# Performance work log

Measured on AMD Instinct MI355X. Metric: run time of the kernel, lower is better.

## Reference

```python
import jax, jax.numpy as jnp
import numpy as np

EPS = 1e-5
GROUPS = 8
NUM_HEADS = 8


def setup_inputs() -> dict:
    key = jax.random.key(0)
    ks = jax.random.split(key, 6)
    C = 512
    s = 1.0 / np.sqrt(C)
    return {
        "x": jax.random.normal(ks[0], (8, C, 32, 32), dtype=jnp.float32),
        "gn_w": jnp.ones((C,), jnp.float32),
        "gn_b": jnp.zeros((C,), jnp.float32),
        "wq": jax.random.normal(ks[1], (C, C), jnp.float32) * s,
        "bq": jnp.zeros((C,), jnp.float32),
        "wk": jax.random.normal(ks[2], (C, C), jnp.float32) * s,
        "bk": jnp.zeros((C,), jnp.float32),
        "wv": jax.random.normal(ks[3], (C, C), jnp.float32) * s,
        "bv": jnp.zeros((C,), jnp.float32),
        "wp": jax.random.normal(ks[4], (C, C), jnp.float32) * s,
        "bp": jnp.zeros((C,), jnp.float32),
    }


def _group_norm(x, w, b):
    # x: [B, C, H, W]; normalize per group over (C//G, H, W)
    B, C, H, W = x.shape
    xg = x.reshape(B, GROUPS, -1)
    mean = xg.mean(axis=-1, keepdims=True)
    var = xg.var(axis=-1, keepdims=True)
    xn = ((xg - mean) * jax.lax.rsqrt(var + EPS)).reshape(B, C, H, W)
    return xn * w[None, :, None, None] + b[None, :, None, None]


def reference(x, gn_w, gn_b, wq, bq, wk, bk, wv, bv, wp, bp):
    B, C, H, W = x.shape
    n_heads = NUM_HEADS
    d = C // n_heads
    scale = 1.0 / np.sqrt(d)

    x_flat = x.reshape(B, C, H * W).transpose(0, 2, 1)       # [B, S, C]
    xn = _group_norm(x, gn_w, gn_b).reshape(B, C, H * W).transpose(0, 2, 1)

    # torch Linear: y = x @ W.T + b
    q = (xn @ wq.T + bq).reshape(B, H * W, n_heads, d)        # [B, S, h, d]
    k = (xn @ wk.T + bk).reshape(B, H * W, n_heads, d)
    v = (xn @ wv.T + bv).reshape(B, H * W, n_heads, d)

    attn = jnp.einsum("bnhd,bmhd->bhnm", q, k) * scale       # [B, h, S, S]
    attn = jax.nn.softmax(attn, axis=-1)
    out = jnp.einsum("bhnm,bmhd->bnhd", attn, v).reshape(B, H * W, C)
    out = out @ wp.T + bp
    out = out + x_flat
    return out.transpose(0, 2, 1).reshape(B, C, H, W)
```

## Files before the change

### kernel.cpp

```cpp
#include <hip/hip_runtime.h>
#include <stdint.h>

typedef unsigned short u16;
using bf16x8 = __attribute__((ext_vector_type(8))) short;
using f32x4  = __attribute__((ext_vector_type(4))) float;
using f32x16 = __attribute__((ext_vector_type(16))) float;
typedef unsigned int uv2 __attribute__((ext_vector_type(2)));

#define EPS_GN 1e-5f
#define SCL 0.18033688011112042f

__device__ __forceinline__ u16 f2bf(float f) {
  union { float f; uint32_t u; } x; x.f = f;
  uint32_t r = x.u + 0x7FFFu + ((x.u >> 16) & 1u);
  return (u16)(r >> 16);
}

__device__ __forceinline__ void gload_lds16(const void* g, void* l) {
  __builtin_amdgcn_global_load_lds(
      (const __attribute__((address_space(1))) unsigned int*)g,
      (__attribute__((address_space(3))) unsigned int*)l, 16, 0, 0);
}

__device__ __forceinline__ void fence_tile() {
  asm volatile("s_waitcnt vmcnt(0)" ::: "memory");
  __builtin_amdgcn_s_barrier();
  __builtin_amdgcn_sched_barrier(0);
}

__global__ __launch_bounds__(256) void prep(const float* __restrict__ x,
    float* __restrict__ part,
    const float4* __restrict__ wq, const float4* __restrict__ wk,
    const float4* __restrict__ wv, const float4* __restrict__ wp,
    const float* __restrict__ bq, const float* __restrict__ bk,
    const float* __restrict__ bv,
    u16* __restrict__ wqkv, u16* __restrict__ wpb, float* __restrict__ bqkv) {
  if (blockIdx.x < 512) {
    int bg = blockIdx.x >> 3, seg = blockIdx.x & 7;
    const float4* base = (const float4*)(x + (size_t)bg * 65536 + (size_t)seg * 8192);
    float s = 0.f, s2 = 0.f;
    for (int i = threadIdx.x; i < 2048; i += 256) {
      float4 v = base[i];
      s  += v.x + v.y + v.z + v.w;
      s2 += v.x*v.x + v.y*v.y + v.z*v.z + v.w*v.w;
    }
    for (int m = 1; m < 64; m <<= 1) { s += __shfl_xor(s, m); s2 += __shfl_xor(s2, m); }
    __shared__ float red[4][2];
    int wave = threadIdx.x >> 6;
    if ((threadIdx.x & 63) == 0) { red[wave][0] = s; red[wave][1] = s2; }
    __syncthreads();
    if (threadIdx.x == 0) {
      float a = 0.f, b = 0.f;
      for (int w = 0; w < 4; ++w) { a += red[w][0]; b += red[w][1]; }
      part[blockIdx.x * 2] = a; part[blockIdx.x * 2 + 1] = b;
    }
  } else {
    int i = (blockIdx.x - 512) * 256 + threadIdx.x;
    int seg = i >> 16, j = i & 65535;
    const float4* w = (seg == 0) ? wq : (seg == 1) ? wk : (seg == 2) ? wv : wp;
    u16* o = (seg < 3) ? (wqkv + seg * 262144) : wpb;
    float sc = (seg == 0) ? SCL : 1.f;
    float4 v = w[j];
    o[j*4+0] = f2bf(v.x*sc); o[j*4+1] = f2bf(v.y*sc);
    o[j*4+2] = f2bf(v.z*sc); o[j*4+3] = f2bf(v.w*sc);
    if (i < 1536) bqkv[i] = (i < 512) ? bq[i]*SCL : (i < 1024) ? bk[i-512] : bv[i-1024];
  }
}

__global__ __launch_bounds__(256) void gn_apply(const float* __restrict__ x,
    const float* __restrict__ part, const float* __restrict__ w,
    const float* __restrict__ bb, u16* __restrict__ xn) {
  __shared__ float t[32][33];
  int s0 = blockIdx.x * 32, c0 = blockIdx.y * 32, b = blockIdx.z;
  int g = c0 >> 6;
  float s = 0.f, s2 = 0.f;
  for (int q = 0; q < 8; ++q) {
    s  += part[((b*8+g)*8 + q)*2];
    s2 += part[((b*8+g)*8 + q)*2 + 1];
  }
  float mean = s * (1.f/65536.f);
  float rstd = rsqrtf(s2 * (1.f/65536.f) - mean*mean + EPS_GN);
  for (int i = 0; i < 4; ++i) {
    int c = c0 + threadIdx.y + i * 8;
    float v = x[((size_t)b*512 + c)*1024 + s0 + threadIdx.x];
    t[threadIdx.y + i*8][threadIdx.x] = (v - mean) * rstd * w[c] + bb[c];
  }
  __syncthreads();
  for (int i = 0; i < 4; ++i) {
    int sdx = s0 + threadIdx.y + i * 8;
    xn[((size_t)b*1024 + sdx)*512 + c0 + threadIdx.x] = f2bf(t[threadIdx.x][threadIdx.y + i*8]);
  }
}

__global__ __launch_bounds__(256) void qkv_gemm(const u16* __restrict__ X,
    const u16* __restrict__ W, const float* __restrict__ bias,
    u16* __restrict__ qkb, u16* __restrict__ vP) {
  __shared__ __align__(16) u16 As[2*64*64];
  __shared__ __align__(16) u16 Bs[2*128*64];
  const int K = 512;
  int m0 = (blockIdx.x & 127) * 64, n0 = (blockIdx.x >> 7) * 128;
  int t = threadIdx.x, lane = t & 63, wave = t >> 6;
  int wm = wave >> 1, wn = wave & 1;
  int lr = lane & 15, lg = lane >> 4;
  f32x4 acc[2][4] = {};

  auto stage = [&](int k0, int bufi) {
    u16* Ab = As + bufi * 4096;
    u16* Bb = Bs + bufi * 8192;
#pragma unroll
    for (int c = 0; c < 2; ++c) {
      int chunk = wave * 2 + c;
      int e = chunk * 512 + lane * 8;
      int r = e >> 6, col = e & 63;
      int scol = col ^ ((r & 7) << 3);
      gload_lds16(X + (size_t)(m0 + r) * K + k0 + scol, (char*)Ab + chunk * 1024);
    }
#pragma unroll
    for (int c = 0; c < 4; ++c) {
      int chunk = wave * 4 + c;
      int e = chunk * 512 + lane * 8;
      int r = e >> 6, col = e & 63;
      int scol = col ^ ((r & 7) << 3);
      gload_lds16(W + (size_t)(n0 + r) * K + k0 + scol, (char*)Bb + chunk * 1024);
    }
  };

  stage(0, 0);
  fence_tile();
  int buf = 0;
  for (int k0 = 0; k0 < K; k0 += 64) {
    if (k0 + 64 < K) stage(k0 + 64, buf ^ 1);
    const char* Ab = (const char*)(As + buf * 4096);
    const char* Bb = (const char*)(Bs + buf * 8192);
    bf16x8 af[2][2], bfr[4][2];
#pragma unroll
    for (int kk = 0; kk < 2; ++kk) {
      int ca = kk * 64 + lg * 16;
#pragma unroll
      for (int i = 0; i < 2; ++i) {
        int ra = wm * 32 + i * 16 + lr;
        af[i][kk] = *(const bf16x8*)(Ab + ((ra * 128 + ca) ^ ((ra & 7) << 4)));
      }
#pragma unroll
      for (int j = 0; j < 4; ++j) {
        int rb = wn * 64 + j * 16 + lr;
        bfr[j][kk] = *(const bf16x8*)(Bb + ((rb * 128 + ca) ^ ((rb & 7) << 4)));
      }
    }
    __builtin_amdgcn_s_setprio(1);
#pragma unroll
    for (int kk = 0; kk < 2; ++kk)
#pragma unroll
      for (int i = 0; i < 2; ++i)
#pragma unroll
        for (int j = 0; j < 4; ++j)
          acc[i][j] = __builtin_amdgcn_mfma_f32_16x16x32_bf16(af[i][kk], bfr[j][kk], acc[i][j], 0, 0, 0);
    __builtin_amdgcn_s_setprio(0);
    fence_tile();
    buf ^= 1;
  }
  if (n0 < 1024) {
    for (int i = 0; i < 2; ++i)
      for (int j = 0; j < 4; ++j) {
        int col = n0 + wn * 64 + j * 16 + lr;
        float bv = bias[col];
        int rowb = m0 + wm * 32 + i * 16 + lg * 4;
        for (int r = 0; r < 4; ++r)
          qkb[(size_t)(rowb + r) * 1024 + col] = f2bf(acc[i][j][r] + bv);
      }
  } else {
    for (int i = 0; i < 2; ++i)
      for (int j = 0; j < 4; ++j) {
        int col = n0 + wn * 64 + j * 16 + lr;
        float bv = bias[col];
        int rowb = m0 + wm * 32 + i * 16 + lg * 4;
        int colV = col - 1024;
        int h  = colV >> 6, dl = colV & 63;
        int dt = dl >> 5,  lqv = dl & 31;
        int bb2 = rowb >> 10, s_in = rowb & 1023;
        int tile = s_in >> 6, kvl = s_in & 63;
        int cg = kvl >> 4, hiv = (kvl >> 3) & 1, j0 = kvl & 7;
        int ii = dt * 4 + cg, lv = hiv * 32 + lqv;
        size_t u16off = ((size_t)((h * 8 + bb2) * 16 + tile)) * 4096 + (ii * 64 + lv) * 8 + j0;
        unsigned p0, p1;
        float v0 = acc[i][j][0] + bv, v1 = acc[i][j][1] + bv;
        float v2 = acc[i][j][2] + bv, v3 = acc[i][j][3] + bv;
        asm("v_cvt_pk_bf16_f32 %0, %1, %2" : "=v"(p0) : "v"(v0), "v"(v1));
        asm("v_cvt_pk_bf16_f32 %0, %1, %2" : "=v"(p1) : "v"(v2), "v"(v3));
        uint2 pk; pk.x = p0; pk.y = p1;
        *(uint2*)(vP + u16off) = pk;
      }
  }
}

__global__ __launch_bounds__(256) void proj_gemm(const u16* __restrict__ Wt,
    const u16* __restrict__ X, const float* __restrict__ bias,
    const float* __restrict__ resid, float* __restrict__ Out) {
  __shared__ __align__(16) u16 As[2*128*64];
  __shared__ __align__(16) u16 Bs[2*64*64];
  const int K = 512;
  int m0 = blockIdx.x * 64, n0 = blockIdx.y * 128;
  int t = threadIdx.x, lane = t & 63, wave = t >> 6;
  int wm = wave >> 1, wn = wave & 1;
  int lr = lane & 15, lg = lane >> 4;
  f32x4 acc[4][2] = {};

  auto stage = [&](int k0, int bufi) {
    u16* Ab = As + bufi * 8192;
    u16* Bb = Bs + bufi * 4096;
#pragma unroll
    for (int c = 0; c < 4; ++c) {
      int chunk = wave * 4 + c;
      int e = chunk * 512 + lane * 8;
      int r = e >> 6, col = e & 63;
      int scol = col ^ ((r & 7) << 3);
      gload_lds16(Wt + (size_t)(n0 + r) * K + k0 + scol, (char*)Ab + chunk * 1024);
    }
#pragma unroll
    for (int c = 0; c < 2; ++c) {
      int chunk = wave * 2 + c;
      int e = chunk * 512 + lane * 8;
      int r = e >> 6, col = e & 63;
      int scol = col ^ ((r & 7) << 3);
      gload_lds16(X + (size_t)(m0 + r) * K + k0 + scol, (char*)Bb + chunk * 1024);
    }
  };

  stage(0, 0);
  fence_tile();
  int buf = 0;
  for (int k0 = 0; k0 < K; k0 += 64) {
    if (k0 + 64 < K) stage(k0 + 64, buf ^ 1);
    const char* Ab = (const char*)(As + buf * 8192);
    const char* Bb = (const char*)(Bs + buf * 4096);
    bf16x8 af[4][2], bfr[2][2];
#pragma unroll
    for (int kk = 0; kk < 2; ++kk) {
      int ca = kk * 64 + lg * 16;
#pragma unroll
      for (int i = 0; i < 4; ++i) {
        int ra = wm * 64 + i * 16 + lr;
        af[i][kk] = *(const bf16x8*)(Ab + ((ra * 128 + ca) ^ ((ra & 7) << 4)));
      }
#pragma unroll
      for (int j = 0; j < 2; ++j) {
        int rb = wn * 32 + j * 16 + lr;
        bfr[j][kk] = *(const bf16x8*)(Bb + ((rb * 128 + ca) ^ ((rb & 7) << 4)));
      }
    }
    __builtin_amdgcn_s_setprio(1);
#pragma unroll
    for (int kk = 0; kk < 2; ++kk)
#pragma unroll
      for (int i = 0; i < 4; ++i)
#pragma unroll
        for (int j = 0; j < 2; ++j)
          acc[i][j] = __builtin_amdgcn_mfma_f32_16x16x32_bf16(af[i][kk], bfr[j][kk], acc[i][j], 0, 0, 0);
    __builtin_amdgcn_s_setprio(0);
    fence_tile();
    buf ^= 1;
  }
  for (int i = 0; i < 4; ++i)
    for (int j = 0; j < 2; ++j) {
      int mcol = m0 + wn * 32 + j * 16 + lr;
      for (int r = 0; r < 4; ++r) {
        int nrow = n0 + wm * 64 + i * 16 + lg * 4 + r;
        float v = acc[i][j][r] + bias[nrow];
        size_t b = (size_t)(mcol >> 10); int s = mcol & 1023;
        size_t addr = (b * 512 + nrow) * 1024 + s;
        Out[addr] = v + resid[addr];
      }
    }
}

__global__ __launch_bounds__(512, 4) void attn_fwd(const u16* __restrict__ qk,
    const u16* __restrict__ vP, u16* __restrict__ o) {
  __shared__ __align__(16) u16 smem[26624];
  int bh = blockIdx.x, qb = blockIdx.y;
  int b = bh >> 3, h = bh & 7;
  int t = threadIdx.x, lane = t & 63, wave = t >> 6;
  int half = wave >> 2, wq4 = wave & 3;
  int lq = lane & 31, hi = lane >> 5;
  int qrow0 = qb * 128 + wq4 * 32;
  const u16* qp = qk + (size_t)(b * 1024 + qrow0 + lq) * 1024 + h * 64 + hi * 8;
  bf16x8 qf[4];
#pragma unroll
  for (int s = 0; s < 4; ++s) qf[s] = *(const bf16x8*)(qp + s * 16);
  float li = 0.f;
  f32x16 ot[2] = {};
  int kvbase = half * 512;
  const u16* vb = vP + ((size_t)((h * 8 + b) * 16 + half * 8)) * 4096 + (size_t)lane * 8;

  auto stage = [&](int ti, int bufi) {
    u16* Kb = smem + (half * 2 + bufi) * 4096;
    int kv = kvbase + ti * 64;
#pragma unroll
    for (int c = 0; c < 2; ++c) {
      int chunk = wq4 * 2 + c;
      int e = chunk * 512 + lane * 8;
      int r = e >> 6, col = e & 63;
      int scol = col ^ ((r & 7) << 3);
      gload_lds16(qk + (size_t)(b * 1024 + kv + r) * 1024 + 512 + h * 64 + scol,
                  (char*)Kb + chunk * 1024);
    }
  };

  stage(0, 0);
  fence_tile();
  int buf = 0;
  for (int ti = 0; ti < 8; ++ti) {
    if (ti < 7) stage(ti + 1, buf ^ 1);
    const char* Kb = (const char*)(smem + (half * 2 + buf) * 4096);
    f32x16 st[2];
#pragma unroll
    for (int n2 = 0; n2 < 2; ++n2) {
      int rk = n2 * 32 + lq;
      f32x16 z = {};
      __builtin_amdgcn_s_setprio(1);
#pragma unroll
      for (int s = 0; s < 4; ++s) {
        bf16x8 kf = *(const bf16x8*)(Kb + ((rk * 128 + s * 32 + hi * 16) ^ ((rk & 7) << 4)));
        z = __builtin_amdgcn_mfma_f32_32x32x16_bf16(kf, qf[s], z, 0, 0, 0);
      }
      __builtin_amdgcn_s_setprio(0);
      st[n2] = z;
    }
    float sm[16];
#pragma unroll
    for (int r = 0; r < 16; ++r) {
      float e0 = __builtin_amdgcn_exp2f(st[0][r]);
      float e1 = __builtin_amdgcn_exp2f(st[1][r]);
      st[0][r] = e0; st[1][r] = e1;
      sm[r] = e0 + e1;
    }
#pragma unroll
    for (int s = 8; s > 0; s >>= 1)
#pragma unroll
      for (int r = 0; r < s; ++r) sm[r] += sm[r + s];
    li += sm[0] + __shfl_xor(sm[0], 32);
    bf16x8 fr[4];
#pragma unroll
    for (int n2 = 0; n2 < 2; ++n2) {
#pragma unroll
      for (int c = 0; c < 2; ++c) {
        unsigned W0, W1, W2, W3;
        asm("v_cvt_pk_bf16_f32 %0, %1, %2" : "=v"(W0) : "v"(st[n2][8*c+0]), "v"(st[n2][8*c+1]));
        asm("v_cvt_pk_bf16_f32 %0, %1, %2" : "=v"(W1) : "v"(st[n2][8*c+2]), "v"(st[n2][8*c+3]));
        asm("v_cvt_pk_bf16_f32 %0, %1, %2" : "=v"(W2) : "v"(st[n2][8*c+4]), "v"(st[n2][8*c+5]));
        asm("v_cvt_pk_bf16_f32 %0, %1, %2" : "=v"(W3) : "v"(st[n2][8*c+6]), "v"(st[n2][8*c+7]));
        uv2 r02 = __builtin_amdgcn_permlane32_swap(W0, W2, false, false);
        uv2 r13 = __builtin_amdgcn_permlane32_swap(W1, W3, false, false);
        union { unsigned u[4]; bf16x8 v; } f;
        f.u[0] = r02[0]; f.u[1] = r13[0]; f.u[2] = r02[1]; f.u[3] = r13[1];
        fr[n2 * 2 + c] = f.v;
      }
    }
    bf16x8 vr[8];
#pragma unroll
    for (int i = 0; i < 8; ++i) vr[i] = *(const bf16x8*)(vb + ti * 4096 + i * 512);
    __builtin_amdgcn_s_setprio(1);
#pragma unroll
    for (int cg = 0; cg < 4; ++cg)
#pragma unroll
      for (int dt = 0; dt < 2; ++dt)
        ot[dt] = __builtin_amdgcn_mfma_f32_32x32x16_bf16(vr[dt * 4 + cg], fr[cg], ot[dt], 0, 0, 0);
    __builtin_amdgcn_s_setprio(0);
    fence_tile();
    buf ^= 1;
  }
  float* cbuf = (float*)smem;
  float* wreg = cbuf + wq4 * 2176;
  if (half == 0) {
#pragma unroll
    for (int dt = 0; dt < 2; ++dt)
#pragma unroll
      for (int r = 0; r < 16; ++r)
        wreg[(dt * 16 + r) * 64 + lane] = ot[dt][r];
    wreg[2048 + lane] = li;
  }
  __syncthreads();
  if (half == 1) {
    float inv = 1.f / (wreg[2048 + lane] + li);
    u16* wb = smem + 18432 + wq4 * 2048;
#pragma unroll
    for (int dt = 0; dt < 2; ++dt)
#pragma unroll
      for (int g = 0; g < 4; ++g) {
        float v0 = (wreg[(dt*16 + 4*g+0)*64 + lane] + ot[dt][4*g+0]) * inv;
        float v1 = (wreg[(dt*16 + 4*g+1)*64 + lane] + ot[dt][4*g+1]) * inv;
        float v2 = (wreg[(dt*16 + 4*g+2)*64 + lane] + ot[dt][4*g+2]) * inv;
        float v3 = (wreg[(dt*16 + 4*g+3)*64 + lane] + ot[dt][4*g+3]) * inv;
        unsigned p0, p1;
        asm("v_cvt_pk_bf16_f32 %0, %1, %2" : "=v"(p0) : "v"(v0), "v"(v1));
        asm("v_cvt_pk_bf16_f32 %0, %1, %2" : "=v"(p1) : "v"(v2), "v"(v3));
        int ch = dt * 8 + 2 * g + hi;
        int pos = ch ^ ((lq & 7) << 1);
        uint2 wv; wv.x = p0; wv.y = p1;
        *(uint2*)((char*)wb + lq * 128 + pos * 8) = wv;
      }
    int q2 = lane >> 1, j0 = lane & 1;
#pragma unroll
    for (int jj = 0; jj < 4; ++jj) {
      int j = j0 + jj * 2;
      uint4 val = *(const uint4*)((const char*)wb + q2 * 128 + ((j ^ (q2 & 7)) << 4));
      *(uint4*)(o + (size_t)(b * 1024 + qrow0 + q2) * 512 + h * 64 + j * 8) = val;
    }
  }
}

extern "C" void kernel_launch(void* const* d_in, const int* in_sizes, int n_in,
                              void* d_out, int out_size, void* d_ws, size_t ws_size,
                              hipStream_t stream) {
  const float* x    = (const float*)d_in[0];
  const float* gn_w = (const float*)d_in[1];
  const float* gn_b = (const float*)d_in[2];
  const float* wq   = (const float*)d_in[3];
  const float* bq   = (const float*)d_in[4];
  const float* wk   = (const float*)d_in[5];
  const float* bk   = (const float*)d_in[6];
  const float* wv   = (const float*)d_in[7];
  const float* bv   = (const float*)d_in[8];
  const float* wp   = (const float*)d_in[9];
  const float* bp   = (const float*)d_in[10];

  char* ws = (char*)d_ws;
  float* part  = (float*)ws;
  float* bqkv  = (float*)(ws + 4096);
  u16* wqkv = (u16*)(ws + 16384);
  u16* wpb  = (u16*)(ws + 1589248);
  u16* xn   = (u16*)(ws + 2113536);
  u16* qkb  = (u16*)(ws + 10502144);
  u16* vPb  = (u16*)(ws + 27279360);
  u16* attno = xn;

  prep<<<1536, 256, 0, stream>>>(x, part,
      (const float4*)wq, (const float4*)wk, (const float4*)wv, (const float4*)wp,
      bq, bk, bv, wqkv, wpb, bqkv);
  gn_apply<<<dim3(32, 16, 8), dim3(32, 8), 0, stream>>>(x, part, gn_w, gn_b, xn);
  qkv_gemm<<<1536, 256, 0, stream>>>(xn, wqkv, bqkv, qkb, vPb);
  attn_fwd<<<dim3(64, 8), 512, 0, stream>>>(qkb, vPb, attno);
  proj_gemm<<<dim3(128, 4), 256, 0, stream>>>(wpb, attno, bp, x, (float*)d_out);
}
```

Baseline: 73.40 us.

## Pre-pack K into MFMA fragment layout and load directly from global in attention

After: 74.34 us. About the same (+1.3%).

```diff
diff --git a/kernel.cpp b/kernel.cpp
--- a/kernel.cpp
+++ b/kernel.cpp
@@ -94,7 +94,7 @@
 
 __global__ __launch_bounds__(256) void qkv_gemm(const u16* __restrict__ X,
     const u16* __restrict__ W, const float* __restrict__ bias,
-    u16* __restrict__ qkb, u16* __restrict__ vP) {
+    u16* __restrict__ qb, u16* __restrict__ kP, u16* __restrict__ vP) {
   __shared__ __align__(16) u16 As[2*64*64];
   __shared__ __align__(16) u16 Bs[2*128*64];
   const int K = 512;
@@ -159,14 +159,30 @@
     fence_tile();
     buf ^= 1;
   }
-  if (n0 < 1024) {
+  if (n0 < 512) {
     for (int i = 0; i < 2; ++i)
       for (int j = 0; j < 4; ++j) {
         int col = n0 + wn * 64 + j * 16 + lr;
         float bv = bias[col];
         int rowb = m0 + wm * 32 + i * 16 + lg * 4;
         for (int r = 0; r < 4; ++r)
-          qkb[(size_t)(rowb + r) * 1024 + col] = f2bf(acc[i][j][r] + bv);
+          qb[(size_t)(rowb + r) * 512 + col] = f2bf(acc[i][j][r] + bv);
+      }
+  } else if (n0 < 1024) {
+    for (int i = 0; i < 2; ++i)
+      for (int j = 0; j < 4; ++j) {
+        int col = n0 + wn * 64 + j * 16 + lr;
+        float bv = bias[col];
+        int colK = col - 512;
+        int h = colK >> 6, dcol = colK & 63;
+        int s = dcol >> 4, hi2 = (dcol >> 3) & 1, jj = dcol & 7;
+        int rowb = m0 + wm * 32 + i * 16 + lg * 4;
+        int bb2 = rowb >> 10, s_in = rowb & 1023;
+        int tile = s_in >> 6, kvl = s_in & 63;
+        int n2 = kvl >> 5, lq0 = kvl & 31;
+        size_t base = ((size_t)(((h * 8 + bb2) * 16 + tile) * 8 + n2 * 4 + s)) * 512 + jj;
+        for (int r = 0; r < 4; ++r)
+          kP[base + (size_t)(hi2 * 32 + lq0 + r) * 8] = f2bf(acc[i][j][r] + bv);
       }
   } else {
     for (int i = 0; i < 2; ++i)
@@ -273,55 +289,36 @@
     }
 }
 
-__global__ __launch_bounds__(512, 4) void attn_fwd(const u16* __restrict__ qk,
-    const u16* __restrict__ vP, u16* __restrict__ o) {
+__global__ __launch_bounds__(512, 4) void attn_fwd(const u16* __restrict__ qb,
+    const u16* __restrict__ kP, const u16* __restrict__ vP, u16* __restrict__ o) {
   __shared__ __align__(16) u16 smem[26624];
-  int bh = blockIdx.x, qb = blockIdx.y;
+  int bh = blockIdx.x, qb_i = blockIdx.y;
   int b = bh >> 3, h = bh & 7;
   int t = threadIdx.x, lane = t & 63, wave = t >> 6;
   int half = wave >> 2, wq4 = wave & 3;
   int lq = lane & 31, hi = lane >> 5;
-  int qrow0 = qb * 128 + wq4 * 32;
-  const u16* qp = qk + (size_t)(b * 1024 + qrow0 + lq) * 1024 + h * 64 + hi * 8;
+  int qrow0 = qb_i * 128 + wq4 * 32;
+  const u16* qp = qb + (size_t)(b * 1024 + qrow0 + lq) * 512 + h * 64 + hi * 8;
   bf16x8 qf[4];
 #pragma unroll
   for (int s = 0; s < 4; ++s) qf[s] = *(const bf16x8*)(qp + s * 16);
   float li = 0.f;
   f32x16 ot[2] = {};
-  int kvbase = half * 512;
+  const u16* kb = kP + ((size_t)((h * 8 + b) * 16 + half * 8)) * 4096 + (size_t)lane * 8;
   const u16* vb = vP + ((size_t)((h * 8 + b) * 16 + half * 8)) * 4096 + (size_t)lane * 8;
 
-  auto stage = [&](int ti, int bufi) {
-    u16* Kb = smem + (half * 2 + bufi) * 4096;
-    int kv = kvbase + ti * 64;
-#pragma unroll
-    for (int c = 0; c < 2; ++c) {
-      int chunk = wq4 * 2 + c;
-      int e = chunk * 512 + lane * 8;
-      int r = e >> 6, col = e & 63;
-      int scol = col ^ ((r & 7) << 3);
-      gload_lds16(qk + (size_t)(b * 1024 + kv + r) * 1024 + 512 + h * 64 + scol,
-                  (char*)Kb + chunk * 1024);
-    }
-  };
-
-  stage(0, 0);
-  fence_tile();
-  int buf = 0;
   for (int ti = 0; ti < 8; ++ti) {
-    if (ti < 7) stage(ti + 1, buf ^ 1);
-    const char* Kb = (const char*)(smem + (half * 2 + buf) * 4096);
+    bf16x8 kf[8];
+#pragma unroll
+    for (int f = 0; f < 8; ++f) kf[f] = *(const bf16x8*)(kb + ti * 4096 + f * 512);
     f32x16 st[2];
 #pragma unroll
     for (int n2 = 0; n2 < 2; ++n2) {
-      int rk = n2 * 32 + lq;
       f32x16 z = {};
       __builtin_amdgcn_s_setprio(1);
 #pragma unroll
-      for (int s = 0; s < 4; ++s) {
-        bf16x8 kf = *(const bf16x8*)(Kb + ((rk * 128 + s * 32 + hi * 16) ^ ((rk & 7) << 4)));
-        z = __builtin_amdgcn_mfma_f32_32x32x16_bf16(kf, qf[s], z, 0, 0, 0);
-      }
+      for (int s = 0; s < 4; ++s)
+        z = __builtin_amdgcn_mfma_f32_32x32x16_bf16(kf[n2 * 4 + s], qf[s], z, 0, 0, 0);
       __builtin_amdgcn_s_setprio(0);
       st[n2] = z;
     }
@@ -365,8 +362,6 @@
       for (int dt = 0; dt < 2; ++dt)
         ot[dt] = __builtin_amdgcn_mfma_f32_32x32x16_bf16(vr[dt * 4 + cg], fr[cg], ot[dt], 0, 0, 0);
     __builtin_amdgcn_s_setprio(0);
-    fence_tile();
-    buf ^= 1;
   }
   float* cbuf = (float*)smem;
   float* wreg = cbuf + wq4 * 2176;
@@ -429,7 +424,8 @@
   u16* wqkv = (u16*)(ws + 16384);
   u16* wpb  = (u16*)(ws + 1589248);
   u16* xn   = (u16*)(ws + 2113536);
-  u16* qkb  = (u16*)(ws + 10502144);
+  u16* qb   = (u16*)(ws + 10502144);
+  u16* kPb  = qb + 4194304;
   u16* vPb  = (u16*)(ws + 27279360);
   u16* attno = xn;
 
@@ -437,7 +433,7 @@
       (const float4*)wq, (const float4*)wk, (const float4*)wv, (const float4*)wp,
       bq, bk, bv, wqkv, wpb, bqkv);
   gn_apply<<<dim3(32, 16, 8), dim3(32, 8), 0, stream>>>(x, part, gn_w, gn_b, xn);
-  qkv_gemm<<<1536, 256, 0, stream>>>(xn, wqkv, bqkv, qkb, vPb);
-  attn_fwd<<<dim3(64, 8), 512, 0, stream>>>(qkb, vPb, attno);
+  qkv_gemm<<<1536, 256, 0, stream>>>(xn, wqkv, bqkv, qb, kPb, vPb);
+  attn_fwd<<<dim3(64, 8), 512, 0, stream>>>(qb, kPb, vPb, attno);
   proj_gemm<<<dim3(128, 4), 256, 0, stream>>>(wpb, attno, bp, x, (float*)d_out);
 }
```
